# Optimization experiments

Measured on AMD Instinct MI355X. Metric: run time of the kernel, lower is better.

The kernel has to match this reference:

```python
import jax, jax.numpy as jnp
import numpy as np

# Module hyperparameters (match init_kwargs)
B = 4          # batch
SEQ = 4096     # seq_len
STATE = 128    # state_len
T = SEQ + 2 * STATE   # 4352, divisible by 8 -> no eval-time padding branch
DIN = 512      # dim_input
DK = 64        # dim_key
DV = 64        # dim_value
SCALE = 0.125  # scaling_factor = 1/sqrt(dim_key)


def setup_inputs() -> dict:
    key = jax.random.key(0)
    ks = jax.random.split(key, 7)
    x = jax.random.normal(ks[0], (B, T, DIN), dtype=jnp.float32)
    def w(k, dout):
        # nn.Linear(bias=False) weight, used as x @ W with W:[DIN, dout]
        return jax.random.normal(k, (DIN, dout), dtype=jnp.float32) / np.sqrt(DIN).astype(np.float32)
    return {
        'x': x,
        'Wq': w(ks[1], DK), 'Wk': w(ks[2], DK), 'Wv': w(ks[3], DV),
        'Wq_s': w(ks[4], DK), 'Wk_s': w(ks[5], DK), 'Wv_s': w(ks[6], DV),
    }


def reference(x, Wq, Wk, Wv, Wq_s, Wk_s, Wv_s):
    # extract_state: first state_len tokens, middle seq, last state_len tokens
    x_s0 = x[:, :STATE, :]
    x_mid = x[:, STATE:STATE + SEQ, :]
    x_s1 = x[:, STATE + SEQ:, :]

    # separate projections for state vs sequence tokens, then concat along time
    q = jnp.concatenate([x_s0 @ Wq_s, x_mid @ Wq, x_s1 @ Wq_s], axis=1)  # [B,T,DK]
    k = jnp.concatenate([x_s0 @ Wk_s, x_mid @ Wk, x_s1 @ Wk_s], axis=1)  # [B,T,DK]
    v = jnp.concatenate([x_s0 @ Wv_s, x_mid @ Wv, x_s1 @ Wv_s], axis=1)  # [B,T,DV]

    # tril(ones).log() -> 0 on/below diagonal, -inf above (causal log-mask)
    causal = jnp.tril(jnp.ones((T, T), dtype=bool))
    attn_bias = jnp.where(causal, jnp.float32(0.0), -jnp.inf)  # [T,T], broadcast over batch

    scores = jnp.einsum('btd,bsd->bts', q, k) * jnp.float32(SCALE) + attn_bias  # [B,T,T]
    att = jax.nn.softmax(scores, axis=-1)
    out = jnp.einsum('bts,bsd->btd', att, v)  # [B,T,DV]
    return out
```

## Files before the change

### kernel.cpp

```cpp
#include <hip/hip_runtime.h>
#include <hip/hip_bf16.h>

#define TT    4352
#define NBATCH 4
#define DD    64
#define DIN_  512
#define NQT   68
#define MAXC  9
#define CHUNK 8
#define LOG2E 1.44269504f
#define M0B   8.65617025f

typedef _Float16 h4 __attribute__((ext_vector_type(4)));
typedef _Float16 h8 __attribute__((ext_vector_type(8)));
typedef float    f4 __attribute__((ext_vector_type(4)));

__global__ void prep_w_k(const float* __restrict__ Wq, const float* __restrict__ Wk,
                         const float* __restrict__ Wv, const float* __restrict__ Wqs,
                         const float* __restrict__ Wks, const float* __restrict__ Wvs,
                         _Float16* __restrict__ WT, _Float16* __restrict__ WTs) {
  const int n = blockIdx.x;
  const int k = threadIdx.x;
  const bool sflag = (n >= 192);
  const int nn = sflag ? n - 192 : n;
  const int m = nn >> 6;
  const int c = nn & 63;
  const float* src = sflag ? (m == 0 ? Wqs : (m == 1 ? Wks : Wvs))
                           : (m == 0 ? Wq  : (m == 1 ? Wk  : Wv));
  float v = src[k * DD + c];
  if (m == 0) v *= 0.125f;
  (sflag ? WTs : WT)[nn * DIN_ + k] = (_Float16)v;
}

__global__ __launch_bounds__(64) void qkv_proj_k(
    const float* __restrict__ x, const _Float16* __restrict__ WT,
    const _Float16* __restrict__ WTs, _Float16* __restrict__ Q,
    _Float16* __restrict__ K, _Float16* __restrict__ V2) {
  const int g0 = blockIdx.x * 16;
  const int t0 = g0 % TT;
  const int bb = g0 / TT;
  const int lane = threadIdx.x & 63;
  const int l15  = lane & 15;
  const int g4   = lane >> 4;

  const bool use_s = (t0 < 128) || (t0 >= 4224);
  const _Float16* __restrict__ Wsel = use_s ? WTs : WT;

  h8 xf[16];
#pragma unroll
  for (int ks = 0; ks < 16; ++ks) {
    const float* xp = x + (size_t)(g0 + l15) * DIN_ + 32 * ks + 8 * g4;
    f4 a0 = *(const f4*)xp;
    f4 a1 = *(const f4*)(xp + 4);
#pragma unroll
    for (int i = 0; i < 4; ++i) { xf[ks][i] = (_Float16)a0[i]; xf[ks][4 + i] = (_Float16)a1[i]; }
  }

#define WLOAD(dst, kss)                                                        \
  {                                                                            \
    _Pragma("unroll") for (int j = 0; j < 4; ++j) dst[j] =                     \
        *(const h8*)(Wb + (size_t)(16 * j + l15) * DIN_ + 32 * (kss) + 8 * g4);\
  }

#pragma unroll
  for (int oid = 0; oid < 3; ++oid) {
    const _Float16* __restrict__ Wb = Wsel + (size_t)oid * 64 * DIN_;
    h8 w0[4], w1[4], w2[4], w3[4];
    WLOAD(w0, 0) WLOAD(w1, 1) WLOAD(w2, 2) WLOAD(w3, 3)
    f4 acc[4] = {};
#pragma unroll
    for (int ks = 0; ks < 16; ks += 4) {
#pragma unroll
      for (int j = 0; j < 4; ++j)
        acc[j] = __builtin_amdgcn_mfma_f32_16x16x32_f16(xf[ks], w0[j], acc[j], 0, 0, 0);
      if (ks + 4 < 16) WLOAD(w0, ks + 4)
#pragma unroll
      for (int j = 0; j < 4; ++j)
        acc[j] = __builtin_amdgcn_mfma_f32_16x16x32_f16(xf[ks + 1], w1[j], acc[j], 0, 0, 0);
      if (ks + 5 < 16) WLOAD(w1, ks + 5)
#pragma unroll
      for (int j = 0; j < 4; ++j)
        acc[j] = __builtin_amdgcn_mfma_f32_16x16x32_f16(xf[ks + 2], w2[j], acc[j], 0, 0, 0);
      if (ks + 6 < 16) WLOAD(w2, ks + 6)
#pragma unroll
      for (int j = 0; j < 4; ++j)
        acc[j] = __builtin_amdgcn_mfma_f32_16x16x32_f16(xf[ks + 3], w3[j], acc[j], 0, 0, 0);
      if (ks + 7 < 16) WLOAD(w3, ks + 7)
    }

    if (oid == 0) {
#pragma unroll
      for (int j = 0; j < 4; ++j)
#pragma unroll
        for (int r = 0; r < 4; ++r)
          Q[(size_t)(g0 + 4 * g4 + r) * DD + 16 * j + l15] = (_Float16)acc[j][r];
    } else if (oid == 1) {
#pragma unroll
      for (int j = 0; j < 4; ++j)
#pragma unroll
        for (int r = 0; r < 4; ++r)
          K[(size_t)(g0 + 4 * g4 + r) * DD + 16 * j + l15] = (_Float16)acc[j][r];
    } else {
      const int kvt = t0 >> 6;
      const int jj  = (t0 >> 4) & 3;
      _Float16* vt = V2 + (size_t)(bb * NQT + kvt) * 4096;
#pragma unroll
      for (int j = 0; j < 4; ++j) {
        h4 pk;
#pragma unroll
        for (int r = 0; r < 4; ++r) pk[r] = (_Float16)acc[j][r];
        const int u = (16 * j + l15) * 8 + (jj >> 1) * 4 + g4;
        *(h4*)(vt + (size_t)u * 8 + (jj & 1) * 4) = pk;
      }
    }
  }
#undef WLOAD
}

static __device__ __forceinline__ void lds_put(char* base, int u, h8 v) {
  const int row = u >> 3, cc = u & 7;
  *(h8*)(base + row * 128 + ((cc ^ (row & 7)) << 4)) = v;
}

__global__ __launch_bounds__(256) void attn_part_k(
    const _Float16* __restrict__ Q, const _Float16* __restrict__ K,
    const _Float16* __restrict__ V2, float* __restrict__ Op,
    float* __restrict__ Lp) {
  const int bid = blockIdx.x;
  const int b   = bid & 3;
  const int r   = bid >> 2;
  const int c   = r % MAXC;
  const int qt  = NQT - 1 - r / MAXC;
  const int n   = qt + 1;
  const int tb  = c * CHUNK;
  const int te  = min(tb + CHUNK, n);
  if (tb >= te) return;

  const int tid  = threadIdx.x;
  const int w    = tid >> 6;
  const int lane = tid & 63;
  const int l15  = lane & 15;
  const int g4   = lane >> 4;
  const int qrow_in = w * 16 + l15;
  const int qrow    = qt * 64 + qrow_in;

  __shared__ __align__(16) char lds[2][16384];

  const _Float16* Qp  = Q + (size_t)(b * TT + qrow) * DD + 8 * g4;
  const _Float16* Kb  = K + (size_t)b * TT * DD;
  const _Float16* V2b = V2 + (size_t)b * NQT * 4096;

  const h8 qf0 = *(const h8*)Qp;
  const h8 qf1 = *(const h8*)(Qp + 32);

  f4 o[4] = {};
  f4 ls = {0.f, 0.f, 0.f, 0.f};

  const int u1 = tid, u2 = tid + 256;
  const int sw0 = (g4 ^ (l15 & 7)) << 4;
  const int sw1 = ((g4 + 4) ^ (l15 & 7)) << 4;

  {
    const _Float16* Ks = Kb + (size_t)tb * (64 * DD);
    const _Float16* Vs = V2b + (size_t)tb * 4096;
    h8 k1 = *(const h8*)(Ks + (size_t)u1 * 8);
    h8 k2 = *(const h8*)(Ks + (size_t)u2 * 8);
    h8 v1 = *(const h8*)(Vs + (size_t)u1 * 8);
    h8 v2 = *(const h8*)(Vs + (size_t)u2 * 8);
    lds_put(lds[0], u1, k1);        lds_put(lds[0], u2, k2);
    lds_put(lds[0] + 8192, u1, v1); lds_put(lds[0] + 8192, u2, v2);
  }
  __syncthreads();

  int cur = 0;
  for (int t = tb; t < te; ++t) {
    const bool have = (t + 1 < te);
    h8 k1, k2, v1, v2;
    if (have) {
      const _Float16* Ks = Kb + (size_t)(t + 1) * (64 * DD);
      const _Float16* Vs = V2b + (size_t)(t + 1) * 4096;
      k1 = *(const h8*)(Ks + (size_t)u1 * 8);
      k2 = *(const h8*)(Ks + (size_t)u2 * 8);
      v1 = *(const h8*)(Vs + (size_t)u1 * 8);
      v2 = *(const h8*)(Vs + (size_t)u2 * 8);
    }
    char* Kl = lds[cur];
    char* Vl = lds[cur] + 8192;
    f4 s[4] = {};
#pragma unroll
    for (int j = 0; j < 4; ++j) {
      const int rb = (16 * j + l15) * 128;
      h8 ka = *(const h8*)(Kl + rb + sw0);
      h8 kb = *(const h8*)(Kl + rb + sw1);
      s[j] = __builtin_amdgcn_mfma_f32_16x16x32_f16(ka, qf0, s[j], 0, 0, 0);
      s[j] = __builtin_amdgcn_mfma_f32_16x16x32_f16(kb, qf1, s[j], 0, 0, 0);
    }
    if (t == qt) {
#pragma unroll
      for (int j = 0; j < 4; ++j)
#pragma unroll
        for (int rr = 0; rr < 4; ++rr)
          if (16 * j + 4 * g4 + rr > qrow_in) s[j][rr] = -1e30f;
    }
    h8 pa0, pa1;
#pragma unroll
    for (int j = 0; j < 4; ++j)
#pragma unroll
      for (int rr = 0; rr < 4; ++rr) {
        float p = exp2f(fmaf(s[j][rr], LOG2E, -M0B));
        ls[rr] += p;
        if (j < 2) pa0[(j & 1) * 4 + rr] = (_Float16)p;
        else       pa1[(j & 1) * 4 + rr] = (_Float16)p;
      }
#pragma unroll
    for (int j = 0; j < 4; ++j) {
      const int rb = (16 * j + l15) * 128;
      h8 va = *(const h8*)(Vl + rb + sw0);
      h8 vb = *(const h8*)(Vl + rb + sw1);
      o[j] = __builtin_amdgcn_mfma_f32_16x16x32_f16(va, pa0, o[j], 0, 0, 0);
      o[j] = __builtin_amdgcn_mfma_f32_16x16x32_f16(vb, pa1, o[j], 0, 0, 0);
    }
    if (have) {
      char* Kn = lds[cur ^ 1];
      lds_put(Kn, u1, k1);        lds_put(Kn, u2, k2);
      lds_put(Kn + 8192, u1, v1); lds_put(Kn + 8192, u2, v2);
    }
    __syncthreads();
    cur ^= 1;
  }

  float lrow = ls[0] + ls[1] + ls[2] + ls[3];
  lrow += __shfl_xor(lrow, 16, 64);
  lrow += __shfl_xor(lrow, 32, 64);

  const int pb = (b * NQT + qt) * MAXC + c;
  float* op = Op + (size_t)pb * 4096 + w * 1024;
#pragma unroll
  for (int j = 0; j < 4; ++j)
    *(f4*)(op + (j * 64 + lane) * 4) = o[j];
  if (g4 == 0)
    Lp[pb * 64 + w * 16 + l15] = lrow;
}

__global__ __launch_bounds__(256) void attn_comb_k(
    const float* __restrict__ Op, const float* __restrict__ Lp,
    float* __restrict__ out) {
  const int bq = blockIdx.x;
  const int b = bq / NQT, qt = bq % NQT;
  const int tid  = threadIdx.x;
  const int w    = tid >> 6;
  const int lane = tid & 63;
  const int l15  = lane & 15;
  const int g4   = lane >> 4;
  const int n = qt + 1;
  const int pb0 = (b * NQT + qt) * MAXC;

  f4 o[4] = {};
  float lrow = 0.f;
#pragma unroll
  for (int c = 0; c < MAXC; ++c) {
    if (c * CHUNK >= n) break;
    const int pb = pb0 + c;
    lrow += Lp[pb * 64 + w * 16 + l15];
    const float* op = Op + (size_t)pb * 4096 + w * 1024;
#pragma unroll
    for (int j = 0; j < 4; ++j)
      o[j] += *(const f4*)(op + (j * 64 + lane) * 4);
  }

  const float inv = 1.f / lrow;
  float* dst = out + (size_t)(b * TT + qt * 64 + w * 16 + l15) * DD + 4 * g4;
#pragma unroll
  for (int j = 0; j < 4; ++j) {
    f4 res = { o[j][0] * inv, o[j][1] * inv, o[j][2] * inv, o[j][3] * inv };
    *(f4*)(dst + 16 * j) = res;
  }
}

extern "C" void kernel_launch(void* const* d_in, const int* in_sizes, int n_in,
                              void* d_out, int out_size, void* d_ws, size_t ws_size,
                              hipStream_t stream) {
  const float* x   = (const float*)d_in[0];
  const float* Wq  = (const float*)d_in[1];
  const float* Wk  = (const float*)d_in[2];
  const float* Wv  = (const float*)d_in[3];
  const float* Wqs = (const float*)d_in[4];
  const float* Wks = (const float*)d_in[5];
  const float* Wvs = (const float*)d_in[6];
  float* out = (float*)d_out;

  char* ws = (char*)d_ws;
  const size_t WT_BYTES = (size_t)192 * DIN_ * sizeof(_Float16);
  const size_t QK_BYTES = (size_t)NBATCH * TT * DD * sizeof(_Float16);
  const size_t OP_BYTES = (size_t)NBATCH * NQT * MAXC * 4096 * sizeof(float);
  _Float16* WT  = (_Float16*)(ws);
  _Float16* WTs = (_Float16*)(ws + WT_BYTES);
  _Float16* Qh  = (_Float16*)(ws + 2 * WT_BYTES);
  _Float16* Kh  = (_Float16*)(ws + 2 * WT_BYTES + QK_BYTES);
  _Float16* V2h = (_Float16*)(ws + 2 * WT_BYTES + 2 * QK_BYTES);
  float*    Op  = (float*)(ws + 2 * WT_BYTES + 3 * QK_BYTES);
  float*    Lp  = (float*)(ws + 2 * WT_BYTES + 3 * QK_BYTES + OP_BYTES);

  hipLaunchKernelGGL(prep_w_k, dim3(384), dim3(512), 0, stream,
                     Wq, Wk, Wv, Wqs, Wks, Wvs, WT, WTs);
  hipLaunchKernelGGL(qkv_proj_k, dim3(NBATCH * TT / 16), dim3(64), 0, stream,
                     x, WT, WTs, Qh, Kh, V2h);
  hipLaunchKernelGGL(attn_part_k, dim3(NBATCH * NQT * MAXC), dim3(256), 0, stream,
                     Qh, Kh, V2h, Op, Lp);
  hipLaunchKernelGGL(attn_comb_k, dim3(NBATCH * NQT), dim3(256), 0, stream,
                     Op, Lp, out);
}
```

Measured before the change: 148.5 us.

## Share projection weights via LDS across 4 waves and store partials in fp16

The QKV projection kernel now runs 64-row blocks of 4 waves. Each wave handles a 16-row tile, and the weight slices are staged once per block in double-buffered LDS with a register prefetch, instead of every single-wave block reading all weights from global memory. Separately, the unnormalized partial attention outputs are written and read as fp16 rather than fp32, halving split-K partial traffic between the partial and combine kernels. Costs are a __syncthreads per k-step in the projection and extra rounding error on the partial sums, since those sums are unnormalized.

```diff
diff --git a/kernel.cpp b/kernel.cpp
--- a/kernel.cpp
+++ b/kernel.cpp
@@ -32,89 +32,91 @@
   (sflag ? WTs : WT)[nn * DIN_ + k] = (_Float16)v;
 }
 
-__global__ __launch_bounds__(64) void qkv_proj_k(
+__global__ __launch_bounds__(256, 2) void qkv_proj_k(
     const float* __restrict__ x, const _Float16* __restrict__ WT,
     const _Float16* __restrict__ WTs, _Float16* __restrict__ Q,
     _Float16* __restrict__ K, _Float16* __restrict__ V2) {
-  const int g0 = blockIdx.x * 16;
-  const int t0 = g0 % TT;
-  const int bb = g0 / TT;
-  const int lane = threadIdx.x & 63;
+  __shared__ __align__(16) _Float16 wlds[2][2048];
+  const int g0  = blockIdx.x * 64;
+  const int t0g = g0 % TT;
+  const int bb  = g0 / TT;
+  const int tid = threadIdx.x;
+  const int w    = tid >> 6;
+  const int lane = tid & 63;
   const int l15  = lane & 15;
   const int g4   = lane >> 4;
-
-  const bool use_s = (t0 < 128) || (t0 >= 4224);
+  const int row0 = g0 + 16 * w;
+
+  const bool use_s = (t0g < 128) || (t0g >= 4224);
   const _Float16* __restrict__ Wsel = use_s ? WTs : WT;
 
   h8 xf[16];
 #pragma unroll
   for (int ks = 0; ks < 16; ++ks) {
-    const float* xp = x + (size_t)(g0 + l15) * DIN_ + 32 * ks + 8 * g4;
+    const float* xp = x + (size_t)(row0 + l15) * DIN_ + 32 * ks + 8 * g4;
     f4 a0 = *(const f4*)xp;
     f4 a1 = *(const f4*)(xp + 4);
 #pragma unroll
     for (int i = 0; i < 4; ++i) { xf[ks][i] = (_Float16)a0[i]; xf[ks][4 + i] = (_Float16)a1[i]; }
   }
 
-#define WLOAD(dst, kss)                                                        \
-  {                                                                            \
-    _Pragma("unroll") for (int j = 0; j < 4; ++j) dst[j] =                     \
-        *(const h8*)(Wb + (size_t)(16 * j + l15) * DIN_ + 32 * (kss) + 8 * g4);\
-  }
-
+  const int sn = tid >> 2, skk = tid & 3;
+
+  h8 wpend, wnew;
+  {
+    h8 w0v = *(const h8*)(Wsel + (size_t)sn * DIN_ + 8 * skk);
+    *(h8*)(&wlds[0][tid * 8]) = w0v;
+    wpend = *(const h8*)(Wsel + (size_t)sn * DIN_ + 32 + 8 * skk);
+  }
+  __syncthreads();
+
+  int cur = 0;
 #pragma unroll
   for (int oid = 0; oid < 3; ++oid) {
-    const _Float16* __restrict__ Wb = Wsel + (size_t)oid * 64 * DIN_;
-    h8 w0[4], w1[4], w2[4], w3[4];
-    WLOAD(w0, 0) WLOAD(w1, 1) WLOAD(w2, 2) WLOAD(w3, 3)
     f4 acc[4] = {};
 #pragma unroll
-    for (int ks = 0; ks < 16; ks += 4) {
+    for (int ks = 0; ks < 16; ++ks) {
+      const int s = oid * 16 + ks;
+      if (s + 2 < 48) {
+        const int o2 = (s + 2) >> 4, k2 = (s + 2) & 15;
+        wnew = *(const h8*)(Wsel + (size_t)(o2 * 64 + sn) * DIN_ + 32 * k2 + 8 * skk);
+      }
+#pragma unroll
+      for (int j = 0; j < 4; ++j) {
+        h8 wj = *(const h8*)(&wlds[cur][((16 * j + l15) * 4 + g4) * 8]);
+        acc[j] = __builtin_amdgcn_mfma_f32_16x16x32_f16(xf[ks], wj, acc[j], 0, 0, 0);
+      }
+      if (s + 1 < 48) *(h8*)(&wlds[cur ^ 1][tid * 8]) = wpend;
+      __syncthreads();
+      wpend = wnew;
+      cur ^= 1;
+    }
+
+    if (oid == 0) {
 #pragma unroll
       for (int j = 0; j < 4; ++j)
-        acc[j] = __builtin_amdgcn_mfma_f32_16x16x32_f16(xf[ks], w0[j], acc[j], 0, 0, 0);
-      if (ks + 4 < 16) WLOAD(w0, ks + 4)
+#pragma unroll
+        for (int r = 0; r < 4; ++r)
+          Q[(size_t)(row0 + 4 * g4 + r) * DD + 16 * j + l15] = (_Float16)acc[j][r];
+    } else if (oid == 1) {
 #pragma unroll
       for (int j = 0; j < 4; ++j)
-        acc[j] = __builtin_amdgcn_mfma_f32_16x16x32_f16(xf[ks + 1], w1[j], acc[j], 0, 0, 0);
-      if (ks + 5 < 16) WLOAD(w1, ks + 5)
-#pragma unroll
-      for (int j = 0; j < 4; ++j)
-        acc[j] = __builtin_amdgcn_mfma_f32_16x16x32_f16(xf[ks + 2], w2[j], acc[j], 0, 0, 0);
-      if (ks + 6 < 16) WLOAD(w2, ks + 6)
-#pragma unroll
-      for (int j = 0; j < 4; ++j)
-        acc[j] = __builtin_amdgcn_mfma_f32_16x16x32_f16(xf[ks + 3], w3[j], acc[j], 0, 0, 0);
-      if (ks + 7 < 16) WLOAD(w3, ks + 7)
-    }
-
-    if (oid == 0) {
-#pragma unroll
-      for (int j = 0; j < 4; ++j)
 #pragma unroll
         for (int r = 0; r < 4; ++r)
-          Q[(size_t)(g0 + 4 * g4 + r) * DD + 16 * j + l15] = (_Float16)acc[j][r];
-    } else if (oid == 1) {
-#pragma unroll
-      for (int j = 0; j < 4; ++j)
-#pragma unroll
-        for (int r = 0; r < 4; ++r)
-          K[(size_t)(g0 + 4 * g4 + r) * DD + 16 * j + l15] = (_Float16)acc[j][r];
+          K[(size_t)(row0 + 4 * g4 + r) * DD + 16 * j + l15] = (_Float16)acc[j][r];
     } else {
-      const int kvt = t0 >> 6;
-      const int jj  = (t0 >> 4) & 3;
+      const int kvt = t0g >> 6;
       _Float16* vt = V2 + (size_t)(bb * NQT + kvt) * 4096;
 #pragma unroll
       for (int j = 0; j < 4; ++j) {
         h4 pk;
 #pragma unroll
         for (int r = 0; r < 4; ++r) pk[r] = (_Float16)acc[j][r];
-        const int u = (16 * j + l15) * 8 + (jj >> 1) * 4 + g4;
-        *(h4*)(vt + (size_t)u * 8 + (jj & 1) * 4) = pk;
+        const int u = (16 * j + l15) * 8 + (w >> 1) * 4 + g4;
+        *(h4*)(vt + (size_t)u * 8 + (w & 1) * 4) = pk;
       }
     }
   }
-#undef WLOAD
 }
 
 static __device__ __forceinline__ void lds_put(char* base, int u, h8 v) {
@@ -124,7 +126,7 @@
 
 __global__ __launch_bounds__(256) void attn_part_k(
     const _Float16* __restrict__ Q, const _Float16* __restrict__ K,
-    const _Float16* __restrict__ V2, float* __restrict__ Op,
+    const _Float16* __restrict__ V2, _Float16* __restrict__ Oph,
     float* __restrict__ Lp) {
   const int bid = blockIdx.x;
   const int b   = bid & 3;
@@ -234,16 +236,20 @@
   lrow += __shfl_xor(lrow, 32, 64);
 
   const int pb = (b * NQT + qt) * MAXC + c;
-  float* op = Op + (size_t)pb * 4096 + w * 1024;
-#pragma unroll
-  for (int j = 0; j < 4; ++j)
-    *(f4*)(op + (j * 64 + lane) * 4) = o[j];
+  _Float16* op = Oph + (size_t)pb * 4096 + w * 1024;
+#pragma unroll
+  for (int j = 0; j < 4; ++j) {
+    h4 pk;
+#pragma unroll
+    for (int rr = 0; rr < 4; ++rr) pk[rr] = (_Float16)o[j][rr];
+    *(h4*)(op + (j * 64 + lane) * 4) = pk;
+  }
   if (g4 == 0)
     Lp[pb * 64 + w * 16 + l15] = lrow;
 }
 
 __global__ __launch_bounds__(256) void attn_comb_k(
-    const float* __restrict__ Op, const float* __restrict__ Lp,
+    const _Float16* __restrict__ Oph, const float* __restrict__ Lp,
     float* __restrict__ out) {
   const int bq = blockIdx.x;
   const int b = bq / NQT, qt = bq % NQT;
@@ -262,10 +268,13 @@
     if (c * CHUNK >= n) break;
     const int pb = pb0 + c;
     lrow += Lp[pb * 64 + w * 16 + l15];
-    const float* op = Op + (size_t)pb * 4096 + w * 1024;
-#pragma unroll
-    for (int j = 0; j < 4; ++j)
-      o[j] += *(const f4*)(op + (j * 64 + lane) * 4);
+    const _Float16* op = Oph + (size_t)pb * 4096 + w * 1024;
+#pragma unroll
+    for (int j = 0; j < 4; ++j) {
+      h4 v = *(const h4*)(op + (j * 64 + lane) * 4);
+#pragma unroll
+      for (int rr = 0; rr < 4; ++rr) o[j][rr] += (float)v[rr];
+    }
   }
 
   const float inv = 1.f / lrow;
@@ -290,23 +299,23 @@
   float* out = (float*)d_out;
 
   char* ws = (char*)d_ws;
-  const size_t WT_BYTES = (size_t)192 * DIN_ * sizeof(_Float16);
-  const size_t QK_BYTES = (size_t)NBATCH * TT * DD * sizeof(_Float16);
-  const size_t OP_BYTES = (size_t)NBATCH * NQT * MAXC * 4096 * sizeof(float);
+  const size_t WT_BYTES  = (size_t)192 * DIN_ * sizeof(_Float16);
+  const size_t QK_BYTES  = (size_t)NBATCH * TT * DD * sizeof(_Float16);
+  const size_t OPH_BYTES = (size_t)NBATCH * NQT * MAXC * 4096 * sizeof(_Float16);
   _Float16* WT  = (_Float16*)(ws);
   _Float16* WTs = (_Float16*)(ws + WT_BYTES);
   _Float16* Qh  = (_Float16*)(ws + 2 * WT_BYTES);
   _Float16* Kh  = (_Float16*)(ws + 2 * WT_BYTES + QK_BYTES);
   _Float16* V2h = (_Float16*)(ws + 2 * WT_BYTES + 2 * QK_BYTES);
-  float*    Op  = (float*)(ws + 2 * WT_BYTES + 3 * QK_BYTES);
-  float*    Lp  = (float*)(ws + 2 * WT_BYTES + 3 * QK_BYTES + OP_BYTES);
+  _Float16* Oph = (_Float16*)(ws + 2 * WT_BYTES + 3 * QK_BYTES);
+  float*    Lp  = (float*)(ws + 2 * WT_BYTES + 3 * QK_BYTES + OPH_BYTES);
 
   hipLaunchKernelGGL(prep_w_k, dim3(384), dim3(512), 0, stream,
                      Wq, Wk, Wv, Wqs, Wks, Wvs, WT, WTs);
-  hipLaunchKernelGGL(qkv_proj_k, dim3(NBATCH * TT / 16), dim3(64), 0, stream,
+  hipLaunchKernelGGL(qkv_proj_k, dim3(NBATCH * TT / 64), dim3(256), 0, stream,
                      x, WT, WTs, Qh, Kh, V2h);
   hipLaunchKernelGGL(attn_part_k, dim3(NBATCH * NQT * MAXC), dim3(256), 0, stream,
-                     Qh, Kh, V2h, Op, Lp);
+                     Qh, Kh, V2h, Oph, Lp);
   hipLaunchKernelGGL(attn_comb_k, dim3(NBATCH * NQT), dim3(256), 0, stream,
-                     Op, Lp, out);
-}
+                     Oph, Lp, out);
+}
```

Result: faster. 134.4 us (-9.5%).
